# Optimization experiments

Hardware: AMD Instinct MI355X
Metric: run time of the kernel (lower is better)

Reference implementation:

```python
import jax, jax.numpy as jnp
import numpy as np
from jax import lax

B, T_PAST, T_FUT, F_IN, F_OUT, H = 512, 128, 48, 64, 16, 512


def setup_inputs() -> dict:
    key = jax.random.key(0)
    ks = jax.random.split(key, 12)
    s = jnp.float32(0.05)
    p = lambda k, shape: jax.random.normal(k, shape, jnp.float32) * s
    return {
        "inp": jax.random.normal(ks[0], (B, T_PAST, F_IN), jnp.float32),
        "target_seq": jax.random.normal(ks[1], (B, T_FUT, F_OUT), jnp.float32),
        "enc1_Wk": p(ks[2], (F_IN, 4 * H)), "enc1_Wr": p(ks[3], (H, 4 * H)), "enc1_b": jnp.zeros((4 * H,), jnp.float32),
        "enc2_Wk": p(ks[4], (H, 4 * H)), "enc2_Wr": p(ks[5], (H, 4 * H)), "enc2_b": jnp.zeros((4 * H,), jnp.float32),
        "dec1_Wk": p(ks[6], (F_OUT, 4 * H)), "dec1_Wr": p(ks[7], (H, 4 * H)), "dec1_b": jnp.zeros((4 * H,), jnp.float32),
        "dec2_Wk": p(ks[8], (H, 4 * H)), "dec2_Wr": p(ks[9], (H, 4 * H)), "dec2_b": jnp.zeros((4 * H,), jnp.float32),
        "fc_W": p(ks[10], (H, F_OUT)), "fc_b": jnp.zeros((F_OUT,), jnp.float32),
    }


def _gates(z, c_prev):
    # Keras gate order: i, f, g(cell), o
    i, f, g, o = jnp.split(z, 4, axis=-1)
    c = jax.nn.sigmoid(f) * c_prev + jax.nn.sigmoid(i) * jnp.tanh(g)
    h = jax.nn.sigmoid(o) * jnp.tanh(c)
    return h, c


def _lstm_layer(xs, h0, c0, Wk, Wr, b):
    # xs: (B, T, D) -> (hs (B,T,H), hT, cT)
    xz = jnp.einsum("btd,dg->btg", xs, Wk) + b  # input projection precomputed
    def step(carry, xz_t):
        h, c = carry
        h2, c2 = _gates(xz_t + h @ Wr, c)
        return (h2, c2), h2
    (hT, cT), hs = lax.scan(step, (h0, c0), jnp.swapaxes(xz, 0, 1))
    return jnp.swapaxes(hs, 0, 1), hT, cT


def reference(inp, target_seq,
              enc1_Wk, enc1_Wr, enc1_b, enc2_Wk, enc2_Wr, enc2_b,
              dec1_Wk, dec1_Wr, dec1_b, dec2_Wk, dec2_Wr, dec2_b,
              fc_W, fc_b):
    b = inp.shape[0]
    z = jnp.zeros((b, H), inp.dtype)
    # Encoder: layer2 initial state = layer1 final state (as in source)
    h1s, h1, c1 = _lstm_layer(inp, z, z, enc1_Wk, enc1_Wr, enc1_b)
    _, h2, c2 = _lstm_layer(h1s, h1, c1, enc2_Wk, enc2_Wr, enc2_b)
    # Decoder: every future step restarts from (h2, c2) with teacher-forced
    # inputs -> steps are independent, compute all in parallel.
    z1 = (jnp.einsum("btf,fg->btg", target_seq, dec1_Wk)
          + (h2 @ dec1_Wr)[:, None, :] + dec1_b)          # (B, Tf, 4H)
    h1d, c1d = _gates(z1, c2[:, None, :])
    # layer2: input = h1d, initial state = (h1d, c1d) (chained per source)
    z2 = jnp.einsum("bth,hg->btg", h1d, dec2_Wk + dec2_Wr) + dec2_b
    h2d, _ = _gates(z2, c1d)
    return jnp.einsum("bth,hf->btf", h2d, fc_W) + fc_b    # (B, Tf, F_OUT)
```

## Files before the change

kernel.cpp:

```cpp
#include <hip/hip_runtime.h>


typedef _Float16 f16;
typedef _Float16 h8 __attribute__((ext_vector_type(8)));
typedef _Float16 h4 __attribute__((ext_vector_type(4)));
typedef _Float16 h2v __attribute__((ext_vector_type(2)));
typedef float f32x4 __attribute__((ext_vector_type(4)));
typedef float f32x2 __attribute__((ext_vector_type(2)));
typedef unsigned long long ull;

#define DEV static __device__ __forceinline__

constexpr int NB   = 512;
constexpr int TP   = 128;
constexpr int TFU  = 48;
constexpr int FIN  = 64;
constexpr int FOUT = 16;
constexpr int HS   = 512;
constexpr int G4   = 2048;

DEV float sigf(float x) { return 1.0f / (1.0f + __expf(-x)); }
DEV float tanh_(float x) { float e = __expf(2.0f * x); return 1.0f - 2.0f / (e + 1.0f); }

DEV void issue_ld(h8& d, const f16* p) {
  asm volatile("global_load_dwordx4 %0, %1, off" : "=v"(d) : "v"(p));
}
DEV void issue_ldc(h8& d, const f16* p) {
  asm volatile("global_load_dwordx4 %0, %1, off sc0 sc1" : "=v"(d) : "v"(p));
}
#define ILDX(dst, base, B) \
  asm volatile("global_load_dwordx4 %0, %1, off offset:" #B : "=v"(dst) : "v"(base));
#define ASM_VM0    asm volatile("s_waitcnt vmcnt(0)" ::: "memory")
#define ASM_VMC(N) asm volatile("s_waitcnt vmcnt(" #N ")" ::: "memory")
#define SBAR       __builtin_amdgcn_sched_barrier(0)

DEV void st_coh_h2(f16* p, h2v v) {
  union { h2v h; unsigned u; } c;
  c.h = v;
  __hip_atomic_store((unsigned*)p, c.u, __ATOMIC_RELAXED, __HIP_MEMORY_SCOPE_AGENT);
}

DEV unsigned xcc_id() {
  unsigned x;
  asm("s_getreg_b32 %0, hwreg(HW_REG_XCC_ID)" : "=s"(x));
  return x & 7;
}

DEV int ic2zc(int ic) { return ((ic >> 4) & 3) * 512 + ((ic >> 6) << 4) + (ic & 15); }

__global__ void k_conv(const float* __restrict__ a, const float* __restrict__ b,
                       f16* __restrict__ a16, f16* __restrict__ b16) {
  const size_t NA = (size_t)NB * TP * FIN;
  const size_t NBT = (size_t)NB * TFU * FOUT;
  for (size_t i = (size_t)blockIdx.x * blockDim.x + threadIdx.x; i < NA + NBT;
       i += (size_t)gridDim.x * blockDim.x) {
    if (i < NA) a16[i] = (f16)a[i];
    else        b16[i - NA] = (f16)b[i - NA];
  }
}

__global__ void k_bias(const float* __restrict__ b1, const float* __restrict__ b2,
                       const float* __restrict__ b3, const float* __restrict__ b4,
                       float* __restrict__ o1, float* __restrict__ o2,
                       float* __restrict__ o3, float* __restrict__ o4) {
  int ic = blockIdx.x * blockDim.x + threadIdx.x;
  if (ic < G4) {
    int zc = ic2zc(ic);
    o1[ic] = b1[zc]; o2[ic] = b2[zc]; o3[ic] = b3[zc]; o4[ic] = b4[zc];
  }
}

__global__ void k_pack(const float* __restrict__ A, const float* __restrict__ Bs,
                       int split, int NKC, int mode, f16* __restrict__ dst) {
  int i = blockIdx.x * blockDim.x + threadIdx.x;
  int total = 128 * NKC * 64;
  if (i >= total) return;
  int lane = i & 63, rem = i >> 6;
  int kc = rem % NKC, nt = rem / NKC;
  int zc = ic2zc(nt * 16 + (lane & 15));
  int k0 = kc * 32 + ((lane >> 4) << 3);
  h8 v;
#pragma unroll
  for (int j = 0; j < 8; j++) {
    int k = k0 + j;
    float x;
    if (mode == 2) x = A[(size_t)k * G4 + zc] + Bs[(size_t)k * G4 + zc];
    else x = (k < split) ? A[(size_t)k * G4 + zc] : Bs[(size_t)(k - split) * G4 + zc];
    v[j] = (f16)x;
  }
  *(h8*)(dst + (size_t)i * 8) = v;
}

__global__ void k_pack_dk16(const float* __restrict__ W, f16* __restrict__ dst) {
  int i = blockIdx.x * blockDim.x + threadIdx.x;
  if (i >= 128 * 64) return;
  int lane = i & 63, nt = i >> 6;
  int zc = ic2zc(nt * 16 + (lane & 15));
  h4 v;
#pragma unroll
  for (int j = 0; j < 4; j++) v[j] = (f16)W[(size_t)(((lane >> 4) << 2) + j) * G4 + zc];
  *(h4*)(dst + (size_t)i * 4) = v;
}

__global__ void k_pack_fc(const float* __restrict__ W, f16* __restrict__ dst) {
  int i = blockIdx.x * blockDim.x + threadIdx.x;
  if (i >= 32 * 64) return;
  int lane = i & 63, q = i >> 6;
  h4 v;
#pragma unroll
  for (int j = 0; j < 4; j++) {
    int k = q * 16 + ((lane >> 4) << 2) + j;
    v[j] = (f16)W[(size_t)k * FOUT + (lane & 15)];
  }
  *(h4*)(dst + (size_t)i * 4) = v;
}

template <int L, bool HIST>
__global__ __launch_bounds__(512, 2) void k_enc(
    const f16* __restrict__ wfrag, const float* __restrict__ biasI,
    f16* __restrict__ h1s, f16* __restrict__ h2r, f16* __restrict__ h2s,
    float* __restrict__ cT, const float* __restrict__ cInit,
    const f16* __restrict__ inp16, unsigned int* __restrict__ cnt,
    int* __restrict__ roster) {
  constexpr int XKC = (L == 1) ? 2 : 16;
  constexpr int NKC = XKC + 16;
  constexpr size_t SLOT = (size_t)NB * HS;
  constexpr bool PLAIN_H = (L == 1) || HIST;

  extern __shared__ __align__(16) char smem[];
  f16* Bl = (f16*)smem;
  float* zl = (float*)(smem + (size_t)NKC * 4096);
  __shared__ int s_gc[2];

  const int tid = threadIdx.x, lane = tid & 63, wid = tid >> 6;
  const int wr4 = wid & 3, wc = wid >> 2;

  if (tid == 0) {
    unsigned x = xcc_id();
    int slot = atomicAdd(&roster[x], 1) & 31;
    s_gc[0] = (int)x; s_gc[1] = slot;
  }
  __syncthreads();
  const int g = s_gc[0], c = s_gc[1];
  const int b0 = g * 64;
  const int l15 = lane & 15, lk = (lane >> 4) << 3;
  const int trow = tid >> 3, tcol = (tid & 7) << 1;

  const int kc0 = ((c >> 1) + 1) & 15;

  {
    const uint4* src = (const uint4*)wfrag + (size_t)c * NKC * 256;
    uint4* dst = (uint4*)smem;
    for (int i = tid; i < NKC * 256; i += 512) dst[i] = src[i];
  }

  float bs[4][2];
#pragma unroll
  for (int ga = 0; ga < 4; ga++) {
    f32x2 bv = *(const f32x2*)(biasI + 64 * c + 16 * ga + tcol);
    bs[ga][0] = bv[0]; bs[ga][1] = bv[1];
  }

  float cst[2];
  if (L == 1) {
    cst[0] = cst[1] = 0.0f;
  } else {
    f32x2 cv = *(const f32x2*)(cInit + (size_t)(b0 + trow) * HS + 16 * c + tcol);
    cst[0] = cv[0]; cst[1] = cv[1];
  }

  const int arow = b0 + 16 * wr4 + l15;

  const f16* bbase[2];
#pragma unroll
  for (int n = 0; n < 2; n++) bbase[n] = Bl + ((size_t)(2 * wc + n) * NKC * 64 + lane) * 8;
  const f16* bh0 = bbase[0] + (size_t)XKC * 512;
  const f16* bh1 = bbase[1] + (size_t)XKC * 512;

  const size_t aoff = ((size_t)(lk >> 4) * 512 + arow) * 16 + (lk & 8);

  unsigned int* cbase = cnt + (size_t)g * TP * 16;

  __syncthreads();

  for (int t = 0; t < TP; t++) {
    h8 ax[XKC];
    if (L == 1) {
      const f16* xb = inp16 + ((size_t)arow * TP + t) * FIN + lk;
      ILDX(ax[0], xb, 0) ILDX(ax[1], xb, 64)
    } else {
      const f16* xp = h1s + (size_t)(t + 1) * SLOT + aoff;
#pragma unroll
      for (int kc = 0; kc < XKC; kc++) {
        issue_ld(ax[kc], xp);
        xp += 16384;
      }
    }
    ASM_VM0; SBAR;

    f32x4 acc[2] = {};
#pragma unroll
    for (int kc = 0; kc < XKC; kc++) {
      h8 bb0 = *(const h8*)(bbase[0] + (size_t)kc * 512);
      h8 bb1 = *(const h8*)(bbase[1] + (size_t)kc * 512);
      acc[0] = __builtin_amdgcn_mfma_f32_16x16x32_f16(ax[kc], bb0, acc[0], 0, 0, 0);
      acc[1] = __builtin_amdgcn_mfma_f32_16x16x32_f16(ax[kc], bb1, acc[1], 0, 0, 0);
    }

    if (t > 0) {
      const unsigned int* cp = cbase + (size_t)(t - 1) * 16;
      while (__hip_atomic_load(cp, __ATOMIC_RELAXED, __HIP_MEMORY_SCOPE_AGENT) < 32u)
        __builtin_amdgcn_s_sleep(1);
      SBAR;
    }

    const f16* hb;
    if (L == 1) hb = h1s + (size_t)t * SLOT;
    else if (HIST) hb = (t == 0) ? (h1s + (size_t)TP * SLOT) : (h2s + (size_t)(t - 1) * SLOT);
    else hb = (t == 0) ? (h1s + (size_t)TP * SLOT) : (h2r + (size_t)((t - 1) & 1) * SLOT);
    const f16* hpb = hb + aoff;

    h8 hA[4], hB[4];
#define LD_H(D, P) { if constexpr (PLAIN_H) issue_ld(D, P); else issue_ldc(D, P); }
#define HB_ISSUE4(R, P)                                                        \
  {                                                                            \
    _Pragma("unroll") for (int j = 0; j < 4; j++) {                            \
      int kk = (kc0 + (P) + j) & 15;                                           \
      const f16* q = hpb + (size_t)kk * 16384;                                 \
      LD_H(R[j], q)                                                            \
    }                                                                          \
  }
#define HB_MFMA4(R, P)                                                         \
  {                                                                            \
    _Pragma("unroll") for (int j = 0; j < 4; j++) {                            \
      int kk = (kc0 + (P) + j) & 15;                                           \
      h8 bb0 = *(const h8*)(bh0 + (size_t)kk * 512);                           \
      h8 bb1 = *(const h8*)(bh1 + (size_t)kk * 512);                           \
      acc[0] = __builtin_amdgcn_mfma_f32_16x16x32_f16(R[j], bb0, acc[0], 0, 0, 0); \
      acc[1] = __builtin_amdgcn_mfma_f32_16x16x32_f16(R[j], bb1, acc[1], 0, 0, 0); \
    }                                                                          \
  }

    HB_ISSUE4(hA, 0)
    HB_ISSUE4(hB, 4)
    ASM_VMC(4); SBAR;
    HB_MFMA4(hA, 0)
    HB_ISSUE4(hA, 8)
    ASM_VMC(4); SBAR;
    HB_MFMA4(hB, 4)
    HB_ISSUE4(hB, 12)
    ASM_VMC(4); SBAR;
    HB_MFMA4(hA, 8)
    ASM_VMC(0); SBAR;
    HB_MFMA4(hB, 12)
#undef HB_ISSUE4
#undef HB_MFMA4
#undef LD_H

#pragma unroll
    for (int n = 0; n < 2; n++) {
      int zr = 16 * wr4 + ((lane >> 4) << 2);
      int zc_ = 32 * wc + 16 * n + l15;
#pragma unroll
      for (int r = 0; r < 4; r++) zl[(size_t)(zr + r) * 68 + zc_] = acc[n][r];
    }
    __syncthreads();

    h2v hv;
    {
      const float* zrow = zl + (size_t)trow * 68 + tcol;
      f32x2 z0 = *(const f32x2*)(zrow + 0);
      f32x2 z1 = *(const f32x2*)(zrow + 16);
      f32x2 z2 = *(const f32x2*)(zrow + 32);
      f32x2 z3 = *(const f32x2*)(zrow + 48);
#pragma unroll
      for (int jj = 0; jj < 2; jj++) {
        float zi = z0[jj] + bs[0][jj];
        float zf = z1[jj] + bs[1][jj];
        float zg = z2[jj] + bs[2][jj];
        float zo = z3[jj] + bs[3][jj];
        float ci = sigf(zf) * cst[jj] + sigf(zi) * tanh_(zg);
        cst[jj] = ci;
        hv[jj] = (f16)(sigf(zo) * tanh_(ci));
      }
    }
    {
      f16* hsl;
      if (L == 1) hsl = h1s + (size_t)(t + 1) * SLOT;
      else if (HIST) hsl = h2s + (size_t)t * SLOT;
      else hsl = h2r + (size_t)(t & 1) * SLOT;
      f16* hp = hsl + ((size_t)c * 512 + b0 + trow) * 16 + tcol;
      if constexpr (PLAIN_H) *(h2v*)hp = hv;
      else st_coh_h2(hp, hv);
    }
    if (t == TP - 1) {
      f32x2 cp;
      cp[0] = cst[0]; cp[1] = cst[1];
      *(f32x2*)(cT + (size_t)(b0 + trow) * HS + 16 * c + tcol) = cp;
    }

    ASM_VM0;
    __syncthreads();
    if (tid == 0)
      __hip_atomic_fetch_add(cbase + (size_t)t * 16, 1u, __ATOMIC_RELAXED,
                             __HIP_MEMORY_SCOPE_AGENT);
  }
}

__global__ __launch_bounds__(256) void k_d1(const f16* __restrict__ h2T,
                                            const f16* __restrict__ wF,
                                            const float* __restrict__ bI,
                                            float* __restrict__ u) {
  const int tid = threadIdx.x, lane = tid & 63, wid = tid >> 6;
  const int wr = wid & 1, wc = wid >> 1;
  const int r0 = (blockIdx.x >> 4) * 32, ic0 = (blockIdx.x & 15) * 128;
  const int l15 = lane & 15, lk = (lane >> 4) << 3;
  const int arow = r0 + 16 * wr + l15;
  const f16* abase = h2T + ((size_t)(lk >> 4) * 512 + arow) * 16 + (lk & 8);
  const int nt0 = (ic0 >> 4) + 4 * wc;
  f32x4 acc[4] = {};
#pragma unroll
  for (int kc = 0; kc < 16; kc++) {
    h8 a = *(const h8*)(abase + (size_t)kc * 16384);
#pragma unroll
    for (int n = 0; n < 4; n++) {
      h8 b = *(const h8*)(wF + ((size_t)(nt0 + n) * 16 + kc) * 512 + (size_t)lane * 8);
      acc[n] = __builtin_amdgcn_mfma_f32_16x16x32_f16(a, b, acc[n], 0, 0, 0);
    }
  }
#pragma unroll
  for (int n = 0; n < 4; n++)
#pragma unroll
    for (int r = 0; r < 4; r++) {
      int row = r0 + 16 * wr + ((lane >> 4) << 2) + r;
      int ic = ic0 + 64 * wc + 16 * n + l15;
      u[(size_t)row * G4 + ic] = acc[n][r] + bI[ic];
    }
}

__global__ __launch_bounds__(256, 1) void k_d2(
    const f16* __restrict__ tg16, const f16* __restrict__ wk16F,
    const float* __restrict__ u, const float* __restrict__ c2T,
    const f16* __restrict__ w2F, const float* __restrict__ b2I,
    const f16* __restrict__ fcF, const float* __restrict__ fcb,
    float* __restrict__ out) {
  extern __shared__ __align__(16) char smem[];
  constexpr size_t H1OFF = 0;
  constexpr size_t C1OFF = 65536;
  constexpr size_t H2OFF = 131072;
  constexpr size_t RDOFF = 143360;

  const int tid = threadIdx.x, lane = tid & 63, wid = tid >> 6;
  const int l15 = lane & 15;
  const int r0 = blockIdx.x * 64;

  {
    const int wr = wid & 1, wc = wid >> 1;
    h4 a[2];
#pragma unroll
    for (int m = 0; m < 2; m++)
      a[m] = *(const h4*)(tg16 + (size_t)(r0 + 32 * wr + 16 * m + l15) * FOUT +
                          ((lane >> 4) << 2));
#pragma unroll 1
    for (int hc = 0; hc < 8; hc++) {
      f32x4 acc[2][8] = {};
#pragma unroll
      for (int n = 0; n < 8; n++) {
        int ntg = 16 * hc + 8 * wc + n;
        h4 b = *(const h4*)(wk16F + ((size_t)ntg * 64 + lane) * 4);
        acc[0][n] = __builtin_amdgcn_mfma_f32_16x16x16f16(a[0], b, acc[0][n], 0, 0, 0);
        acc[1][n] = __builtin_amdgcn_mfma_f32_16x16x16f16(a[1], b, acc[1][n], 0, 0, 0);
      }
#pragma unroll
      for (int m = 0; m < 2; m++)
#pragma unroll
        for (int s = 0; s < 2; s++) {
          int qq = 4 * hc + 2 * wc + s;
          int colh = 16 * qq + l15;
          int icb = 256 * hc + 128 * wc + 64 * s + l15;
#pragma unroll
          for (int r = 0; r < 4; r++) {
            int rl = 32 * wr + 16 * m + ((lane >> 4) << 2) + r;
            int grow = r0 + rl;
            int bidx = grow / 48;
            const float* ub = u + (size_t)bidx * G4;
            float zi = acc[m][4 * s + 0][r] + ub[icb];
            float zf = acc[m][4 * s + 1][r] + ub[icb + 16];
            float zg = acc[m][4 * s + 2][r] + ub[icb + 32];
            float zo = acc[m][4 * s + 3][r] + ub[icb + 48];
            float c2v = c2T[(size_t)bidx * HS + colh];
            float c1 = sigf(zf) * c2v + sigf(zi) * tanh_(zg);
            float h1 = sigf(zo) * tanh_(c1);
            size_t hb = (((size_t)rl * 1024) + (size_t)colh * 2) ^ (size_t)((rl & 7) << 4);
            *(f16*)(smem + H1OFF + hb) = (f16)h1;
            *(f16*)(smem + C1OFF + (size_t)rl * 1024 + (size_t)colh * 2) = (f16)c1;
          }
        }
    }
  }
  __syncthreads();

  {
    const int w = wid;
    f32x4 facc[4] = {};
#pragma unroll 1
    for (int sc = 0; sc < 8; sc++) {
      f32x4 acc[4][4] = {};
#pragma unroll
      for (int kc = 0; kc < 16; kc++) {
        h8 a[4];
#pragma unroll
        for (int mt = 0; mt < 4; mt++) {
          int rl = 16 * mt + l15;
          size_t ab = (((size_t)rl * 1024) + (size_t)(kc * 32 + ((lane >> 4) << 3)) * 2) ^
                      (size_t)((rl & 7) << 4);
          a[mt] = *(const h8*)(smem + H1OFF + ab);
        }
#pragma unroll
        for (int n = 0; n < 4; n++) {
          int nt = 32 * w + 4 * sc + n;
          h8 b = *(const h8*)(w2F + ((size_t)nt * 16 + kc) * 512 + (size_t)lane * 8);
#pragma unroll
          for (int mt = 0; mt < 4; mt++)
            acc[mt][n] = __builtin_amdgcn_mfma_f32_16x16x32_f16(a[mt], b, acc[mt][n], 0, 0, 0);
        }
      }
      int qq = 8 * w + sc;
#pragma unroll
      for (int mt = 0; mt < 4; mt++)
#pragma unroll
        for (int r = 0; r < 4; r++) {
          int rl = 16 * mt + ((lane >> 4) << 2) + r;
          int colh = 16 * qq + l15;
          int ic = 512 * w + 64 * sc + l15;
          float zi = acc[mt][0][r] + b2I[ic];
          float zf = acc[mt][1][r] + b2I[ic + 16];
          float zg = acc[mt][2][r] + b2I[ic + 32];
          float zo = acc[mt][3][r] + b2I[ic + 48];
          float c1v = (float)*(const f16*)(smem + C1OFF + (size_t)rl * 1024 + (size_t)colh * 2);
          float cn = sigf(zf) * c1v + sigf(zi) * tanh_(zg);
          float h2v_ = sigf(zo) * tanh_(cn);
          *(f16*)(smem + H2OFF + (size_t)w * 3072 + (size_t)rl * 48 + (size_t)l15 * 2) = (f16)h2v_;
        }
#pragma unroll
      for (int mt = 0; mt < 4; mt++) {
        h4 aa = *(const h4*)(smem + H2OFF + (size_t)w * 3072 + (size_t)(16 * mt + l15) * 48 +
                             ((lane >> 4) << 3));
        h4 bb = *(const h4*)(fcF + ((size_t)qq * 64 + lane) * 4);
        facc[mt] = __builtin_amdgcn_mfma_f32_16x16x16f16(aa, bb, facc[mt], 0, 0, 0);
      }
    }
#pragma unroll
    for (int mt = 0; mt < 4; mt++)
#pragma unroll
      for (int r = 0; r < 4; r++) {
        int rl = 16 * mt + ((lane >> 4) << 2) + r;
        *(float*)(smem + RDOFF + ((size_t)w * 1152 + (size_t)rl * 18 + l15) * 4) = facc[mt][r];
      }
  }
  __syncthreads();

  {
    int rl = tid >> 2, c4 = (tid & 3) * 4;
    f32x4 o;
#pragma unroll
    for (int j = 0; j < 4; j++) {
      float s = 0.0f;
#pragma unroll
      for (int w = 0; w < 4; w++)
        s += *(const float*)(smem + RDOFF + ((size_t)w * 1152 + (size_t)rl * 18 + c4 + j) * 4);
      o[j] = s + fcb[c4 + j];
    }
    *(f32x4*)(out + (size_t)(r0 + rl) * FOUT + c4) = o;
  }
}

extern "C" void kernel_launch(void* const* d_in, const int* in_sizes, int n_in,
                              void* d_out, int out_size, void* d_ws, size_t ws_size,
                              hipStream_t stream) {
  const float* inp     = (const float*)d_in[0];
  const float* target  = (const float*)d_in[1];
  const float* e1Wk    = (const float*)d_in[2];
  const float* e1Wr    = (const float*)d_in[3];
  const float* e1b     = (const float*)d_in[4];
  const float* e2Wk    = (const float*)d_in[5];
  const float* e2Wr    = (const float*)d_in[6];
  const float* e2b     = (const float*)d_in[7];
  const float* d1Wk    = (const float*)d_in[8];
  const float* d1Wr    = (const float*)d_in[9];
  const float* d1b     = (const float*)d_in[10];
  const float* d2Wk    = (const float*)d_in[11];
  const float* d2Wr    = (const float*)d_in[12];
  const float* d2b     = (const float*)d_in[13];
  const float* fcW     = (const float*)d_in[14];
  const float* fcb     = (const float*)d_in[15];
  float* out = (float*)d_out;

  char* ws = (char*)d_ws;
  size_t off = 0;
  auto carve = [&](size_t bytes) { char* p = ws + off; off += bytes; return p; };
  f16*   inp16 = (f16*)carve((size_t)NB * TP * FIN * 2);
  f16*   tg16  = (f16*)carve((size_t)NB * TFU * FOUT * 2);
  f16*   h1s   = (f16*)carve((size_t)(TP + 1) * NB * HS * 2);
  f16*   h2r   = (f16*)carve((size_t)2 * NB * HS * 2);
  float* c1T   = (float*)carve((size_t)NB * HS * 4);
  float* c2T   = (float*)carve((size_t)NB * HS * 4);
  float* ubuf  = (float*)carve((size_t)NB * G4 * 4);
  f16*   Wc1F  = (f16*)carve((size_t)576 * G4 * 2);
  f16*   Wc2F  = (f16*)carve((size_t)1024 * G4 * 2);
  f16*   d1WrF = (f16*)carve((size_t)512 * G4 * 2);
  f16*   W2sF  = (f16*)carve((size_t)512 * G4 * 2);
  f16*   dk16F = (f16*)carve((size_t)16 * G4 * 2);
  f16*   fcWF  = (f16*)carve((size_t)512 * FOUT * 2);
  float* eB1I  = (float*)carve((size_t)G4 * 4);
  float* eB2I  = (float*)carve((size_t)G4 * 4);
  float* dB1I  = (float*)carve((size_t)G4 * 4);
  float* dB2I  = (float*)carve((size_t)G4 * 4);
  unsigned int* cnt1 = (unsigned int*)carve((size_t)8 * TP * 64);
  unsigned int* cnt2 = (unsigned int*)carve((size_t)8 * TP * 64);
  int*   roster = (int*)carve(256);
  const size_t H2S_BYTES = (size_t)TP * NB * HS * 2;
  bool hist = (ws_size >= off + H2S_BYTES);
  f16* h2s = hist ? (f16*)carve(H2S_BYTES) : nullptr;
  (void)n_in; (void)in_sizes; (void)out_size;

  constexpr int LDS_E1 = 18 * 4096 + 64 * 68 * 4;
  constexpr int LDS_E2 = 32 * 4096 + 64 * 68 * 4;
  constexpr int LDS_D2 = 143360 + 18432;
  {
    void (*p1)(const f16*, const float*, f16*, f16*, f16*, float*, const float*, const f16*,
               unsigned int*, int*) = k_enc<1, true>;
    void (*p2a)(const f16*, const float*, f16*, f16*, f16*, float*, const float*, const f16*,
                unsigned int*, int*) = k_enc<2, true>;
    void (*p2b)(const f16*, const float*, f16*, f16*, f16*, float*, const float*, const f16*,
                unsigned int*, int*) = k_enc<2, false>;
    hipFuncSetAttribute((const void*)p1, hipFuncAttributeMaxDynamicSharedMemorySize, LDS_E1);
    hipFuncSetAttribute((const void*)p2a, hipFuncAttributeMaxDynamicSharedMemorySize, LDS_E2);
    hipFuncSetAttribute((const void*)p2b, hipFuncAttributeMaxDynamicSharedMemorySize, LDS_E2);
    hipFuncSetAttribute((const void*)k_d2, hipFuncAttributeMaxDynamicSharedMemorySize, LDS_D2);
  }

  hipMemsetAsync(cnt1, 0, (size_t)2 * 8 * TP * 64 + 256, stream);
  hipMemsetAsync(h1s, 0, (size_t)NB * HS * 2, stream);

  k_conv<<<4096, 256, 0, stream>>>(inp, target, inp16, tg16);
  k_bias<<<8, 256, 0, stream>>>(e1b, e2b, d1b, d2b, eB1I, eB2I, dB1I, dB2I);
  k_pack<<<576, 256, 0, stream>>>(e1Wk, e1Wr, 64, 18, 1, Wc1F);
  k_pack<<<1024, 256, 0, stream>>>(e2Wk, e2Wr, 512, 32, 1, Wc2F);
  k_pack<<<512, 256, 0, stream>>>(d1Wr, d1Wr, 512, 16, 1, d1WrF);
  k_pack<<<512, 256, 0, stream>>>(d2Wk, d2Wr, 0, 16, 2, W2sF);
  k_pack_dk16<<<32, 256, 0, stream>>>(d1Wk, dk16F);
  k_pack_fc<<<8, 256, 0, stream>>>(fcW, fcWF);

  k_enc<1, true><<<256, 512, LDS_E1, stream>>>(Wc1F, eB1I, h1s, h2r, h2s, c1T, nullptr,
                                               inp16, cnt1, roster);
  int* roster2 = roster + 8;
  if (hist)
    k_enc<2, true><<<256, 512, LDS_E2, stream>>>(Wc2F, eB2I, h1s, h2r, h2s, c2T, c1T,
                                                 nullptr, cnt2, roster2);
  else
    k_enc<2, false><<<256, 512, LDS_E2, stream>>>(Wc2F, eB2I, h1s, h2r, h2s, c2T, c1T,
                                                  nullptr, cnt2, roster2);

  const f16* h2T = hist ? (h2s + (size_t)(TP - 1) * NB * HS) : (h2r + (size_t)1 * NB * HS);
  k_d1<<<256, 256, 0, stream>>>(h2T, d1WrF, dB1I, ubuf);
  k_d2<<<384, 256, LDS_D2, stream>>>(tg16, dk16F, ubuf, c2T, W2sF, dB2I, fcWF, fcb, out);
}
```

Measured before the change: 1.258 ms.

## Prefetch next-step input loads and issue all recurrent h loads upfront

The encoder recurrence loop now issues the input-projection loads for step t+1 at the end of step t, after signalling the counter, so they overlap the inter-block wait. Only wave 0 polls the completion counter and a block barrier releases the others, cutting redundant atomic polling. All 16 recurrent h chunks are loaded at once into four register groups, and the x-projection MFMAs run while those loads are in flight. This raises register pressure and may lower occupancy or cause spills. The barrier-based wait also relies on the counter load being ordered for every wave.

Result: slower. 1.405 ms (+11.7%).

```diff
diff --git a/kernel.cpp b/kernel.cpp
--- a/kernel.cpp
+++ b/kernel.cpp
@@ -183,34 +183,31 @@
 
   __syncthreads();
 
+  h8 ax[XKC];
+#define X_ISSUE(TT)                                                            \
+  {                                                                            \
+    if (L == 1) {                                                              \
+      const f16* xb = inp16 + ((size_t)arow * TP + (TT)) * FIN + lk;           \
+      ILDX(ax[0], xb, 0) ILDX(ax[1], xb, 64)                                   \
+    } else {                                                                   \
+      const f16* xp = h1s + (size_t)((TT) + 1) * SLOT + aoff;                  \
+      _Pragma("unroll") for (int kc = 0; kc < XKC; kc++) {                     \
+        issue_ld(ax[kc], xp);                                                  \
+        xp += 16384;                                                           \
+      }                                                                        \
+    }                                                                          \
+  }
+
+  X_ISSUE(0)
+
   for (int t = 0; t < TP; t++) {
-    h8 ax[XKC];
-    if (L == 1) {
-      const f16* xb = inp16 + ((size_t)arow * TP + t) * FIN + lk;
-      ILDX(ax[0], xb, 0) ILDX(ax[1], xb, 64)
-    } else {
-      const f16* xp = h1s + (size_t)(t + 1) * SLOT + aoff;
-#pragma unroll
-      for (int kc = 0; kc < XKC; kc++) {
-        issue_ld(ax[kc], xp);
-        xp += 16384;
+    if (t > 0) {
+      if (wid == 0) {
+        const unsigned int* cp = cbase + (size_t)(t - 1) * 16;
+        while (__hip_atomic_load(cp, __ATOMIC_RELAXED, __HIP_MEMORY_SCOPE_AGENT) < 32u)
+          __builtin_amdgcn_s_sleep(1);
       }
-    }
-    ASM_VM0; SBAR;
-
-    f32x4 acc[2] = {};
-#pragma unroll
-    for (int kc = 0; kc < XKC; kc++) {
-      h8 bb0 = *(const h8*)(bbase[0] + (size_t)kc * 512);
-      h8 bb1 = *(const h8*)(bbase[1] + (size_t)kc * 512);
-      acc[0] = __builtin_amdgcn_mfma_f32_16x16x32_f16(ax[kc], bb0, acc[0], 0, 0, 0);
-      acc[1] = __builtin_amdgcn_mfma_f32_16x16x32_f16(ax[kc], bb1, acc[1], 0, 0, 0);
-    }
-
-    if (t > 0) {
-      const unsigned int* cp = cbase + (size_t)(t - 1) * 16;
-      while (__hip_atomic_load(cp, __ATOMIC_RELAXED, __HIP_MEMORY_SCOPE_AGENT) < 32u)
-        __builtin_amdgcn_s_sleep(1);
+      __syncthreads();
       SBAR;
     }
 
@@ -220,7 +217,7 @@
     else hb = (t == 0) ? (h1s + (size_t)TP * SLOT) : (h2r + (size_t)((t - 1) & 1) * SLOT);
     const f16* hpb = hb + aoff;
 
-    h8 hA[4], hB[4];
+    h8 hA[4], hB[4], hC[4], hD[4];
 #define LD_H(D, P) { if constexpr (PLAIN_H) issue_ld(D, P); else issue_ldc(D, P); }
 #define HB_ISSUE4(R, P)                                                        \
   {                                                                            \
@@ -243,16 +240,28 @@
 
     HB_ISSUE4(hA, 0)
     HB_ISSUE4(hB, 4)
+    HB_ISSUE4(hC, 8)
+    HB_ISSUE4(hD, 12)
+
+    f32x4 acc[2] = {};
+
+    ASM_VMC(16); SBAR;
+#pragma unroll
+    for (int kc = 0; kc < XKC; kc++) {
+      h8 bb0 = *(const h8*)(bbase[0] + (size_t)kc * 512);
+      h8 bb1 = *(const h8*)(bbase[1] + (size_t)kc * 512);
+      acc[0] = __builtin_amdgcn_mfma_f32_16x16x32_f16(ax[kc], bb0, acc[0], 0, 0, 0);
+      acc[1] = __builtin_amdgcn_mfma_f32_16x16x32_f16(ax[kc], bb1, acc[1], 0, 0, 0);
+    }
+
+    ASM_VMC(12); SBAR;
+    HB_MFMA4(hA, 0)
+    ASM_VMC(8); SBAR;
+    HB_MFMA4(hB, 4)
     ASM_VMC(4); SBAR;
-    HB_MFMA4(hA, 0)
-    HB_ISSUE4(hA, 8)
-    ASM_VMC(4); SBAR;
-    HB_MFMA4(hB, 4)
-    HB_ISSUE4(hB, 12)
-    ASM_VMC(4); SBAR;
-    HB_MFMA4(hA, 8)
+    HB_MFMA4(hC, 8)
     ASM_VMC(0); SBAR;
-    HB_MFMA4(hB, 12)
+    HB_MFMA4(hD, 12)
 #undef HB_ISSUE4
 #undef HB_MFMA4
 #undef LD_H
@@ -304,7 +313,10 @@
     if (tid == 0)
       __hip_atomic_fetch_add(cbase + (size_t)t * 16, 1u, __ATOMIC_RELAXED,
                              __HIP_MEMORY_SCOPE_AGENT);
-  }
+
+    if (t + 1 < TP) X_ISSUE(t + 1)
+  }
+#undef X_ISSUE
 }
 
 __global__ __launch_bounds__(256) void k_d1(const f16* __restrict__ h2T,
```

## Split encoder GEMM across waves by K-halves instead of output columns

Applied to the files above, without the earlier changes.

Waves are now partitioned along the reduction dimension: each pair of wave groups computes all four output column tiles over half of the K chunks, for both the input and recurrent projections. Each wave loads half as many h/x fragments from global memory per step and issues fewer wait/issue phases. The two partial sums are combined through LDS with an extra barrier and a read-modify-write pass. This trades more accumulator registers and an additional synchronization for less per-wave global load latency on the serial recurrence path.

Measured after the change: 1.291 ms. 1.03x slower.

```diff
diff --git a/kernel.cpp b/kernel.cpp
--- a/kernel.cpp
+++ b/kernel.cpp
@@ -28,8 +28,6 @@
 DEV void issue_ldc(h8& d, const f16* p) {
   asm volatile("global_load_dwordx4 %0, %1, off sc0 sc1" : "=v"(d) : "v"(p));
 }
-#define ILDX(dst, base, B) \
-  asm volatile("global_load_dwordx4 %0, %1, off offset:" #B : "=v"(dst) : "v"(base));
 #define ASM_VM0    asm volatile("s_waitcnt vmcnt(0)" ::: "memory")
 #define ASM_VMC(N) asm volatile("s_waitcnt vmcnt(" #N ")" ::: "memory")
 #define SBAR       __builtin_amdgcn_sched_barrier(0)
@@ -123,6 +121,7 @@
     const f16* __restrict__ inp16, unsigned int* __restrict__ cnt,
     int* __restrict__ roster) {
   constexpr int XKC = (L == 1) ? 2 : 16;
+  constexpr int XKH = XKC / 2;
   constexpr int NKC = XKC + 16;
   constexpr size_t SLOT = (size_t)NB * HS;
   constexpr bool PLAIN_H = (L == 1) || HIST;
@@ -133,7 +132,7 @@
   __shared__ int s_gc[2];
 
   const int tid = threadIdx.x, lane = tid & 63, wid = tid >> 6;
-  const int wr4 = wid & 3, wc = wid >> 2;
+  const int wr4 = wid & 3, ks = wid >> 2;
 
   if (tid == 0) {
     unsigned x = xcc_id();
@@ -171,11 +170,9 @@
 
   const int arow = b0 + 16 * wr4 + l15;
 
-  const f16* bbase[2];
-#pragma unroll
-  for (int n = 0; n < 2; n++) bbase[n] = Bl + ((size_t)(2 * wc + n) * NKC * 64 + lane) * 8;
-  const f16* bh0 = bbase[0] + (size_t)XKC * 512;
-  const f16* bh1 = bbase[1] + (size_t)XKC * 512;
+  const f16* bbase[4];
+#pragma unroll
+  for (int n = 0; n < 4; n++) bbase[n] = Bl + ((size_t)n * NKC * 64 + lane) * 8;
 
   const size_t aoff = ((size_t)(lk >> 4) * 512 + arow) * 16 + (lk & 8);
 
@@ -184,27 +181,29 @@
   __syncthreads();
 
   for (int t = 0; t < TP; t++) {
-    h8 ax[XKC];
+    h8 ax[XKH];
     if (L == 1) {
-      const f16* xb = inp16 + ((size_t)arow * TP + t) * FIN + lk;
-      ILDX(ax[0], xb, 0) ILDX(ax[1], xb, 64)
+      const f16* xb = inp16 + ((size_t)arow * TP + t) * FIN + lk + ks * 32;
+      issue_ld(ax[0], xb);
     } else {
-      const f16* xp = h1s + (size_t)(t + 1) * SLOT + aoff;
-#pragma unroll
-      for (int kc = 0; kc < XKC; kc++) {
+      const f16* xp = h1s + (size_t)(t + 1) * SLOT + aoff + (size_t)ks * XKH * 16384;
+#pragma unroll
+      for (int kc = 0; kc < XKH; kc++) {
         issue_ld(ax[kc], xp);
         xp += 16384;
       }
     }
     ASM_VM0; SBAR;
 
-    f32x4 acc[2] = {};
-#pragma unroll
-    for (int kc = 0; kc < XKC; kc++) {
-      h8 bb0 = *(const h8*)(bbase[0] + (size_t)kc * 512);
-      h8 bb1 = *(const h8*)(bbase[1] + (size_t)kc * 512);
-      acc[0] = __builtin_amdgcn_mfma_f32_16x16x32_f16(ax[kc], bb0, acc[0], 0, 0, 0);
-      acc[1] = __builtin_amdgcn_mfma_f32_16x16x32_f16(ax[kc], bb1, acc[1], 0, 0, 0);
+    f32x4 acc[4] = {};
+#pragma unroll
+    for (int kc = 0; kc < XKH; kc++) {
+      int kg = ks * XKH + kc;
+#pragma unroll
+      for (int n = 0; n < 4; n++) {
+        h8 bb = *(const h8*)(bbase[n] + (size_t)kg * 512);
+        acc[n] = __builtin_amdgcn_mfma_f32_16x16x32_f16(ax[kc], bb, acc[n], 0, 0, 0);
+      }
     }
 
     if (t > 0) {
@@ -225,7 +224,7 @@
 #define HB_ISSUE4(R, P)                                                        \
   {                                                                            \
     _Pragma("unroll") for (int j = 0; j < 4; j++) {                            \
-      int kk = (kc0 + (P) + j) & 15;                                           \
+      int kk = (kc0 + 8 * ks + (P) + j) & 15;                                  \
       const f16* q = hpb + (size_t)kk * 16384;                                 \
       LD_H(R[j], q)                                                            \
     }                                                                          \
@@ -233,11 +232,11 @@
 #define HB_MFMA4(R, P)                                                         \
   {                                                                            \
     _Pragma("unroll") for (int j = 0; j < 4; j++) {                            \
-      int kk = (kc0 + (P) + j) & 15;                                           \
-      h8 bb0 = *(const h8*)(bh0 + (size_t)kk * 512);                           \
-      h8 bb1 = *(const h8*)(bh1 + (size_t)kk * 512);                           \
-      acc[0] = __builtin_amdgcn_mfma_f32_16x16x32_f16(R[j], bb0, acc[0], 0, 0, 0); \
-      acc[1] = __builtin_amdgcn_mfma_f32_16x16x32_f16(R[j], bb1, acc[1], 0, 0, 0); \
+      int kk = (kc0 + 8 * ks + (P) + j) & 15;                                  \
+      _Pragma("unroll") for (int n = 0; n < 4; n++) {                          \
+        h8 bb = *(const h8*)(bbase[n] + (size_t)(XKC + kk) * 512);             \
+        acc[n] = __builtin_amdgcn_mfma_f32_16x16x32_f16(R[j], bb, acc[n], 0, 0, 0); \
+      }                                                                        \
     }                                                                          \
   }
 
@@ -245,26 +244,36 @@
     HB_ISSUE4(hB, 4)
     ASM_VMC(4); SBAR;
     HB_MFMA4(hA, 0)
-    HB_ISSUE4(hA, 8)
-    ASM_VMC(4); SBAR;
+    ASM_VMC(0); SBAR;
     HB_MFMA4(hB, 4)
-    HB_ISSUE4(hB, 12)
-    ASM_VMC(4); SBAR;
-    HB_MFMA4(hA, 8)
-    ASM_VMC(0); SBAR;
-    HB_MFMA4(hB, 12)
 #undef HB_ISSUE4
 #undef HB_MFMA4
 #undef LD_H
 
-#pragma unroll
-    for (int n = 0; n < 2; n++) {
+    {
       int zr = 16 * wr4 + ((lane >> 4) << 2);
-      int zc_ = 32 * wc + 16 * n + l15;
-#pragma unroll
-      for (int r = 0; r < 4; r++) zl[(size_t)(zr + r) * 68 + zc_] = acc[n][r];
-    }
-    __syncthreads();
+      if (ks == 0) {
+#pragma unroll
+        for (int n = 0; n < 4; n++) {
+          int zc_ = 16 * n + l15;
+#pragma unroll
+          for (int r = 0; r < 4; r++) zl[(size_t)(zr + r) * 68 + zc_] = acc[n][r];
+        }
+      }
+      __syncthreads();
+      if (ks == 1) {
+#pragma unroll
+        for (int n = 0; n < 4; n++) {
+          int zc_ = 16 * n + l15;
+#pragma unroll
+          for (int r = 0; r < 4; r++) {
+            float* p = &zl[(size_t)(zr + r) * 68 + zc_];
+            *p += acc[n][r];
+          }
+        }
+      }
+      __syncthreads();
+    }
 
     h2v hv;
     {
```
